# Performance work log

Measured on AMD Instinct MI355X. Metric: run time of the kernel, lower is better.

Reference implementation:

```python
import jax, jax.numpy as jnp
import numpy as np

N_NODES = 10000
N_EDGES = 640000
CH = 128


def setup_inputs() -> dict:
    key = jax.random.key(0)
    ks = jax.random.split(key, 12)
    inp = {
        "node_feat": jax.random.normal(ks[0], (N_NODES, 118), dtype=jnp.float32),
        "edge_feat": jax.random.normal(ks[1], (N_EDGES, 22), dtype=jnp.float32),
        "src": jax.random.randint(ks[2], (N_EDGES,), 0, N_NODES),
        "dst": jax.random.randint(ks[3], (N_EDGES,), 0, N_NODES),
        "W_node": jax.random.normal(ks[4], (118, CH), dtype=jnp.float32) * 0.05,
        "b_node": jax.random.normal(ks[5], (CH,), dtype=jnp.float32) * 0.05,
        "W_edge": jax.random.normal(ks[6], (22, CH), dtype=jnp.float32) * 0.05,
        "b_edge": jax.random.normal(ks[7], (CH,), dtype=jnp.float32) * 0.05,
        "W_a1": jax.random.normal(ks[8], (2 * CH, CH), dtype=jnp.float32) * 0.05,
        "b_a1": jax.random.normal(ks[9], (CH,), dtype=jnp.float32) * 0.05,
        "W_a2": jax.random.normal(ks[10], (CH, 1), dtype=jnp.float32) * 0.05,
        "b_a2": jax.random.normal(ks[11], (1,), dtype=jnp.float32) * 0.05,
        "layer_num": 3,
    }
    return inp


def reference(node_feat, edge_feat, src, dst, W_node, b_node, W_edge, b_edge,
              W_a1, b_a1, W_a2, b_a2, layer_num):
    # node_map / edge_map (apply_nodes / apply_edges)
    h = node_feat @ W_node + b_node          # [N, C] node hidden
    eh = edge_feat @ W_edge + b_edge         # [E, C] edge hidden (stored on graph, unused by attn)
    e = None
    for _ in range(layer_num):
        # per-edge gather of src/dst hidden, concat -> small 2-layer MLP
        cat = jnp.concatenate([h[src], h[dst]], axis=-1)   # [E, 2C]
        x = jax.nn.leaky_relu(cat @ W_a1 + b_a1)           # torch default slope 0.01
        e = x @ W_a2 + b_a2                                # [E, 1]
    return e
```

## Files before the change

kernel.cpp:

```cpp
#include <hip/hip_runtime.h>
#include <hip/hip_bf16.h>

#define N_NODES 10000
#define N_EDGES 640000
#define CH 128
#define KN 118

typedef _Float16 h2 __attribute__((ext_vector_type(2)));
typedef _Float16 h8 __attribute__((ext_vector_type(8)));
typedef float f32x4 __attribute__((ext_vector_type(4)));

#define H2_OF(v, k) __builtin_shufflevector((v), (v), 2 * (k), 2 * (k) + 1)

__global__ __launch_bounds__(128) void k1_weights(
    const float* __restrict__ Wn, const float* __restrict__ bn,
    const float* __restrict__ Wa1, const float* __restrict__ ba1,
    const float* __restrict__ w2, _Float16* __restrict__ Mt,
    float* __restrict__ V, _Float16* __restrict__ w2h) {
  int c = threadIdx.x;
  int mat = blockIdx.x / 119;
  int i = blockIdx.x % 119;
  if (mat == 2) {
    w2h[c] = (_Float16)w2[c];
#pragma unroll
    for (int cg = c; cg < 256; cg += 128)
#pragma unroll
      for (int p = 118; p < 128; ++p) Mt[cg * 128 + p] = (_Float16)0.f;
    return;
  }
  const float* B = Wa1 + mat * CH * CH;
  const float* a = (i < KN) ? (Wn + i * CH) : bn;
  float acc = 0.f;
#pragma unroll 8
  for (int j = 0; j < CH; ++j) acc = fmaf(a[j], B[j * CH + c], acc);
  int cg = mat * CH + c;
  if (i < KN) {
    Mt[cg * 128 + i] = (_Float16)acc;
  } else {
    if (mat == 1) acc += ba1[c];
    V[cg] = acc;
  }
}

__global__ __launch_bounds__(128) void k2_mfma(
    const float* __restrict__ nf, const _Float16* __restrict__ Mt,
    const float* __restrict__ V, _Float16* __restrict__ T) {
  __shared__ _Float16 Blds[256 * 128];
  int tx = threadIdx.x;

#pragma unroll
  for (int it = 0; it < 32; ++it) {
    int chunk = it * 128 + tx;
    int cg = chunk >> 4;
    int k0 = (chunk & 15) << 3;
    h8 v = *(const h8*)(Mt + cg * 128 + k0);
    *(h8*)(Blds + cg * 128 + (k0 ^ ((cg & 7) << 3))) = v;
  }

  int wave = tx >> 6;
  int lane = tx & 63;
  int m = lane & 15;
  int quad = lane >> 4;
  int nbase = blockIdx.x * 32 + wave * 16;
  int node = nbase + m;
  const float* arow = nf + (size_t)(node < N_NODES ? node : 0) * KN;

  h8 afrag[4];
#pragma unroll
  for (int s = 0; s < 4; ++s) {
#pragma unroll
    for (int j = 0; j < 8; ++j) {
      int k = s * 32 + quad * 8 + j;
      afrag[s][j] = (k < KN) ? (_Float16)arow[k] : (_Float16)0.f;
    }
  }
  __syncthreads();

  f32x4 acc[16];
#pragma unroll
  for (int ct = 0; ct < 16; ++ct) acc[ct] = f32x4{0.f, 0.f, 0.f, 0.f};
  int swz = (m & 7) << 3;
#pragma unroll
  for (int ct = 0; ct < 16; ++ct) {
    const _Float16* brow = Blds + (ct * 16 + m) * 128;
#pragma unroll
    for (int s = 0; s < 4; ++s) {
      h8 b = *(const h8*)(brow + ((s * 32 + quad * 8) ^ swz));
      acc[ct] = __builtin_amdgcn_mfma_f32_16x16x32_f16(afrag[s], b, acc[ct], 0, 0, 0);
    }
  }

#pragma unroll
  for (int ct = 0; ct < 16; ++ct) {
    int cg = ct * 16 + m;
    float bias = V[cg];
    int mat = cg >> 7;
    int cc = cg & (CH - 1);
    int nd0 = nbase + quad * 4;
    _Float16* tp = T + ((size_t)mat * N_NODES + nd0) * CH + cc;
#pragma unroll
    for (int r = 0; r < 4; ++r) {
      if (nd0 + r < N_NODES) tp[(size_t)r * CH] = (_Float16)(acc[ct][r] + bias);
    }
  }
}

__device__ inline float edge_acc8(h8 s, h8 d, h8 w) {
  h8 t = s + d;
  h8 p = t * (_Float16)0.01f;
  h8 u = __builtin_elementwise_max(t, p);
  float acc = 0.f;
  acc = __builtin_amdgcn_fdot2(H2_OF(u, 0), H2_OF(w, 0), acc, false);
  acc = __builtin_amdgcn_fdot2(H2_OF(u, 1), H2_OF(w, 1), acc, false);
  acc = __builtin_amdgcn_fdot2(H2_OF(u, 2), H2_OF(w, 2), acc, false);
  acc = __builtin_amdgcn_fdot2(H2_OF(u, 3), H2_OF(w, 3), acc, false);
  return acc;
}

__global__ __launch_bounds__(256) void k3_edges(
    const int* __restrict__ src, const int* __restrict__ dst,
    const _Float16* __restrict__ S, const _Float16* __restrict__ D,
    const _Float16* __restrict__ w2h, const float* __restrict__ b2,
    float* __restrict__ out) {
  int tid = blockIdx.x * 256 + threadIdx.x;
  int g = tid >> 4;
  int sub = tid & 15;
  int c0 = sub << 3;

  h8 w = *(const h8*)(w2h + c0);
  int4 s4 = *(const int4*)(src + 4 * g);
  int4 d4 = *(const int4*)(dst + 4 * g);

  const _Float16* Sp = S + c0;
  const _Float16* Dp = D + c0;
  h8 sr0 = *(const h8*)(Sp + ((size_t)s4.x << 7));
  h8 dr0 = *(const h8*)(Dp + ((size_t)d4.x << 7));
  h8 sr1 = *(const h8*)(Sp + ((size_t)s4.y << 7));
  h8 dr1 = *(const h8*)(Dp + ((size_t)d4.y << 7));
  h8 sr2 = *(const h8*)(Sp + ((size_t)s4.z << 7));
  h8 dr2 = *(const h8*)(Dp + ((size_t)d4.z << 7));
  h8 sr3 = *(const h8*)(Sp + ((size_t)s4.w << 7));
  h8 dr3 = *(const h8*)(Dp + ((size_t)d4.w << 7));

  float a0 = edge_acc8(sr0, dr0, w);
  float a1 = edge_acc8(sr1, dr1, w);
  float a2 = edge_acc8(sr2, dr2, w);
  float a3 = edge_acc8(sr3, dr3, w);

  float r0 = a0 + __shfl_xor(a0, 1);
  float r1 = a1 + __shfl_xor(a1, 1);
  float r2 = a2 + __shfl_xor(a2, 1);
  float r3 = a3 + __shfl_xor(a3, 1);
  float v1 = (sub & 1) ? r1 : r0;
  float v2 = (sub & 1) ? r3 : r2;
  float t1 = v1 + __shfl_xor(v1, 2);
  float t2 = v2 + __shfl_xor(v2, 2);
  float u = (sub & 2) ? t2 : t1;
  u += __shfl_xor(u, 4);
  u += __shfl_xor(u, 8);

  if (sub < 4) out[4 * g + sub] = u + b2[0];
}

extern "C" void kernel_launch(void* const* d_in, const int* in_sizes, int n_in,
                              void* d_out, int out_size, void* d_ws, size_t ws_size,
                              hipStream_t stream) {
  const float* nf  = (const float*)d_in[0];
  const int*   src = (const int*)d_in[2];
  const int*   dst = (const int*)d_in[3];
  const float* Wn  = (const float*)d_in[4];
  const float* bn  = (const float*)d_in[5];
  const float* Wa1 = (const float*)d_in[8];
  const float* ba1 = (const float*)d_in[9];
  const float* Wa2 = (const float*)d_in[10];
  const float* ba2 = (const float*)d_in[11];
  float* out = (float*)d_out;

  char* ws = (char*)d_ws;
  _Float16* Mt  = (_Float16*)ws;
  float*    V   = (float*)(ws + 256 * 128 * sizeof(_Float16));
  _Float16* w2h = (_Float16*)((char*)V + 256 * sizeof(float));
  _Float16* T   = (_Float16*)((char*)w2h + 128 * sizeof(_Float16));
  _Float16* S = T;
  _Float16* D = T + (size_t)N_NODES * CH;

  k1_weights<<<239, 128, 0, stream>>>(Wn, bn, Wa1, ba1, Wa2, Mt, V, w2h);
  k2_mfma<<<(N_NODES + 31) / 32, 128, 0, stream>>>(nf, Mt, V, T);
  k3_edges<<<(N_EDGES / 4 * 16) / 256, 256, 0, stream>>>(src, dst, S, D, w2h, ba2, out);
}
```

Measured before the change: 145.0 us.

## Split leaky-relu into linear plus abs terms and gather fp8 node projections

Rewrites leaky_relu(t) as 0.505*t + 0.495*|t|. The linear part is folded into per-node scalars P and Q, computed in the node GEMM kernel, so each edge only needs the abs part plus two scalar gathers. The per-node projected features are now stored as fp8 instead of fp16, which halves the random-gather bytes in the edge kernel. An occupancy hint is also added. The trade-off is fp8 quantization error on the abs term.

```diff
diff --git a/kernel.cpp b/kernel.cpp
--- a/kernel.cpp
+++ b/kernel.cpp
@@ -6,22 +6,20 @@
 #define CH 128
 #define KN 118
 
-typedef _Float16 h2 __attribute__((ext_vector_type(2)));
 typedef _Float16 h8 __attribute__((ext_vector_type(8)));
 typedef float f32x4 __attribute__((ext_vector_type(4)));
-
-#define H2_OF(v, k) __builtin_shufflevector((v), (v), 2 * (k), 2 * (k) + 1)
+typedef float v2f __attribute__((ext_vector_type(2)));
 
 __global__ __launch_bounds__(128) void k1_weights(
     const float* __restrict__ Wn, const float* __restrict__ bn,
     const float* __restrict__ Wa1, const float* __restrict__ ba1,
     const float* __restrict__ w2, _Float16* __restrict__ Mt,
-    float* __restrict__ V, _Float16* __restrict__ w2h) {
+    float* __restrict__ V, float* __restrict__ w495) {
   int c = threadIdx.x;
   int mat = blockIdx.x / 119;
   int i = blockIdx.x % 119;
   if (mat == 2) {
-    w2h[c] = (_Float16)w2[c];
+    w495[c] = 0.495f * w2[c];
 #pragma unroll
     for (int cg = c; cg < 256; cg += 128)
 #pragma unroll
@@ -44,7 +42,9 @@
 
 __global__ __launch_bounds__(128) void k2_mfma(
     const float* __restrict__ nf, const _Float16* __restrict__ Mt,
-    const float* __restrict__ V, _Float16* __restrict__ T) {
+    const float* __restrict__ V, const float* __restrict__ w2,
+    unsigned char* __restrict__ T8, float* __restrict__ P,
+    float* __restrict__ Q) {
   __shared__ _Float16 Blds[256 * 128];
   int tx = threadIdx.x;
 
@@ -90,62 +90,92 @@
     }
   }
 
+  float psum[4] = {0.f, 0.f, 0.f, 0.f};
+  float qsum[4] = {0.f, 0.f, 0.f, 0.f};
+  int nd0 = nbase + quad * 4;
 #pragma unroll
   for (int ct = 0; ct < 16; ++ct) {
     int cg = ct * 16 + m;
     float bias = V[cg];
+    float w505 = 0.505f * w2[cg & (CH - 1)];
     int mat = cg >> 7;
-    int cc = cg & (CH - 1);
-    int nd0 = nbase + quad * 4;
-    _Float16* tp = T + ((size_t)mat * N_NODES + nd0) * CH + cc;
+    unsigned char* tp = T8 + ((size_t)mat * N_NODES + nd0) * CH + (cg & (CH - 1));
 #pragma unroll
     for (int r = 0; r < 4; ++r) {
-      if (nd0 + r < N_NODES) tp[(size_t)r * CH] = (_Float16)(acc[ct][r] + bias);
-    }
-  }
-}
-
-__device__ inline float edge_acc8(h8 s, h8 d, h8 w) {
-  h8 t = s + d;
-  h8 p = t * (_Float16)0.01f;
-  h8 u = __builtin_elementwise_max(t, p);
-  float acc = 0.f;
-  acc = __builtin_amdgcn_fdot2(H2_OF(u, 0), H2_OF(w, 0), acc, false);
-  acc = __builtin_amdgcn_fdot2(H2_OF(u, 1), H2_OF(w, 1), acc, false);
-  acc = __builtin_amdgcn_fdot2(H2_OF(u, 2), H2_OF(w, 2), acc, false);
-  acc = __builtin_amdgcn_fdot2(H2_OF(u, 3), H2_OF(w, 3), acc, false);
+      float v = acc[ct][r] + bias;
+      if (mat == 0) psum[r] += w505 * v; else qsum[r] += w505 * v;
+      unsigned q8 = (unsigned)__builtin_amdgcn_cvt_pk_fp8_f32(v, 0.f, 0, false) & 0xffu;
+      if (nd0 + r < N_NODES) tp[(size_t)r * CH] = (unsigned char)q8;
+    }
+  }
+#pragma unroll
+  for (int r = 0; r < 4; ++r) {
+    float ps = psum[r], qs = qsum[r];
+#pragma unroll
+    for (int t = 1; t < 16; t <<= 1) {
+      ps += __shfl_xor(ps, t);
+      qs += __shfl_xor(qs, t);
+    }
+    if (m == r && nd0 + r < N_NODES) {
+      P[nd0 + r] = ps;
+      Q[nd0 + r] = qs;
+    }
+  }
+}
+
+__device__ __forceinline__ float edge_abs8(uint2 sbv, uint2 dbv,
+                                           f32x4 wa, f32x4 wb) {
+  v2f s0 = __builtin_amdgcn_cvt_pk_f32_fp8(sbv.x, false);
+  v2f s1 = __builtin_amdgcn_cvt_pk_f32_fp8(sbv.x, true);
+  v2f s2 = __builtin_amdgcn_cvt_pk_f32_fp8(sbv.y, false);
+  v2f s3 = __builtin_amdgcn_cvt_pk_f32_fp8(sbv.y, true);
+  v2f d0 = __builtin_amdgcn_cvt_pk_f32_fp8(dbv.x, false);
+  v2f d1 = __builtin_amdgcn_cvt_pk_f32_fp8(dbv.x, true);
+  v2f d2 = __builtin_amdgcn_cvt_pk_f32_fp8(dbv.y, false);
+  v2f d3 = __builtin_amdgcn_cvt_pk_f32_fp8(dbv.y, true);
+  float acc;
+  acc = __builtin_fabsf(s0.x + d0.x) * wa.x;
+  acc = fmaf(__builtin_fabsf(s0.y + d0.y), wa.y, acc);
+  acc = fmaf(__builtin_fabsf(s1.x + d1.x), wa.z, acc);
+  acc = fmaf(__builtin_fabsf(s1.y + d1.y), wa.w, acc);
+  acc = fmaf(__builtin_fabsf(s2.x + d2.x), wb.x, acc);
+  acc = fmaf(__builtin_fabsf(s2.y + d2.y), wb.y, acc);
+  acc = fmaf(__builtin_fabsf(s3.x + d3.x), wb.z, acc);
+  acc = fmaf(__builtin_fabsf(s3.y + d3.y), wb.w, acc);
   return acc;
 }
 
-__global__ __launch_bounds__(256) void k3_edges(
+__global__ __launch_bounds__(256, 8) void k3_edges(
     const int* __restrict__ src, const int* __restrict__ dst,
-    const _Float16* __restrict__ S, const _Float16* __restrict__ D,
-    const _Float16* __restrict__ w2h, const float* __restrict__ b2,
+    const unsigned char* __restrict__ S8, const unsigned char* __restrict__ D8,
+    const float* __restrict__ w495, const float* __restrict__ P,
+    const float* __restrict__ Q, const float* __restrict__ b2,
     float* __restrict__ out) {
   int tid = blockIdx.x * 256 + threadIdx.x;
   int g = tid >> 4;
   int sub = tid & 15;
   int c0 = sub << 3;
 
-  h8 w = *(const h8*)(w2h + c0);
+  f32x4 wa = *(const f32x4*)(w495 + c0);
+  f32x4 wb = *(const f32x4*)(w495 + c0 + 4);
   int4 s4 = *(const int4*)(src + 4 * g);
   int4 d4 = *(const int4*)(dst + 4 * g);
 
-  const _Float16* Sp = S + c0;
-  const _Float16* Dp = D + c0;
-  h8 sr0 = *(const h8*)(Sp + ((size_t)s4.x << 7));
-  h8 dr0 = *(const h8*)(Dp + ((size_t)d4.x << 7));
-  h8 sr1 = *(const h8*)(Sp + ((size_t)s4.y << 7));
-  h8 dr1 = *(const h8*)(Dp + ((size_t)d4.y << 7));
-  h8 sr2 = *(const h8*)(Sp + ((size_t)s4.z << 7));
-  h8 dr2 = *(const h8*)(Dp + ((size_t)d4.z << 7));
-  h8 sr3 = *(const h8*)(Sp + ((size_t)s4.w << 7));
-  h8 dr3 = *(const h8*)(Dp + ((size_t)d4.w << 7));
-
-  float a0 = edge_acc8(sr0, dr0, w);
-  float a1 = edge_acc8(sr1, dr1, w);
-  float a2 = edge_acc8(sr2, dr2, w);
-  float a3 = edge_acc8(sr3, dr3, w);
+  const unsigned char* Sp = S8 + c0;
+  const unsigned char* Dp = D8 + c0;
+  uint2 sb0 = *(const uint2*)(Sp + ((unsigned)s4.x << 7));
+  uint2 db0 = *(const uint2*)(Dp + ((unsigned)d4.x << 7));
+  uint2 sb1 = *(const uint2*)(Sp + ((unsigned)s4.y << 7));
+  uint2 db1 = *(const uint2*)(Dp + ((unsigned)d4.y << 7));
+  uint2 sb2 = *(const uint2*)(Sp + ((unsigned)s4.z << 7));
+  uint2 db2 = *(const uint2*)(Dp + ((unsigned)d4.z << 7));
+  uint2 sb3 = *(const uint2*)(Sp + ((unsigned)s4.w << 7));
+  uint2 db3 = *(const uint2*)(Dp + ((unsigned)d4.w << 7));
+
+  float a0 = edge_abs8(sb0, db0, wa, wb);
+  float a1 = edge_abs8(sb1, db1, wa, wb);
+  float a2 = edge_abs8(sb2, db2, wa, wb);
+  float a3 = edge_abs8(sb3, db3, wa, wb);
 
   float r0 = a0 + __shfl_xor(a0, 1);
   float r1 = a1 + __shfl_xor(a1, 1);
@@ -159,7 +189,11 @@
   u += __shfl_xor(u, 4);
   u += __shfl_xor(u, 8);
 
-  if (sub < 4) out[4 * g + sub] = u + b2[0];
+  if (sub < 4) {
+    int si = sub == 0 ? s4.x : sub == 1 ? s4.y : sub == 2 ? s4.z : s4.w;
+    int di = sub == 0 ? d4.x : sub == 1 ? d4.y : sub == 2 ? d4.z : d4.w;
+    out[4 * g + sub] = u + P[si] + Q[di] + b2[0];
+  }
 }
 
 extern "C" void kernel_launch(void* const* d_in, const int* in_sizes, int n_in,
@@ -177,14 +211,16 @@
   float* out = (float*)d_out;
 
   char* ws = (char*)d_ws;
-  _Float16* Mt  = (_Float16*)ws;
-  float*    V   = (float*)(ws + 256 * 128 * sizeof(_Float16));
-  _Float16* w2h = (_Float16*)((char*)V + 256 * sizeof(float));
-  _Float16* T   = (_Float16*)((char*)w2h + 128 * sizeof(_Float16));
-  _Float16* S = T;
-  _Float16* D = T + (size_t)N_NODES * CH;
-
-  k1_weights<<<239, 128, 0, stream>>>(Wn, bn, Wa1, ba1, Wa2, Mt, V, w2h);
-  k2_mfma<<<(N_NODES + 31) / 32, 128, 0, stream>>>(nf, Mt, V, T);
-  k3_edges<<<(N_EDGES / 4 * 16) / 256, 256, 0, stream>>>(src, dst, S, D, w2h, ba2, out);
-}
+  _Float16* Mt   = (_Float16*)ws;
+  float*    V    = (float*)(ws + 65536);
+  float*    w495 = (float*)(ws + 66560);
+  float*    P    = (float*)(ws + 67072);
+  float*    Q    = (float*)(ws + 107072);
+  unsigned char* T8 = (unsigned char*)(ws + 147072);
+  unsigned char* S8 = T8;
+  unsigned char* D8 = T8 + (size_t)N_NODES * CH;
+
+  k1_weights<<<239, 128, 0, stream>>>(Wn, bn, Wa1, ba1, Wa2, Mt, V, w495);
+  k2_mfma<<<(N_NODES + 31) / 32, 128, 0, stream>>>(nf, Mt, V, Wa2, T8, P, Q);
+  k3_edges<<<(N_EDGES / 4 * 16) / 256, 256, 0, stream>>>(src, dst, S8, D8, w495, P, Q, ba2, out);
+}
```

New measurement: 142.9 us. Within noise of the previous version (-1.4%).
